# Optimization experiments

Hardware: AMD Instinct MI355X
Metric: run time of the kernel (lower is better)

## Reference

```python
import jax, jax.numpy as jnp
import numpy as np

N = 100000      # nodes
E = 1600000     # directed edges (avg degree 16)
DIN, DH, DOUT = 128, 128, 64


def gcn_conv(x, W, b, src, dst, n):
    """PyG GCNConv: out = D^{-1/2} (A + I) D^{-1/2} (x @ W) + b.
    src/dst already include self-loops."""
    deg = jax.ops.segment_sum(jnp.ones_like(src, dtype=x.dtype), dst, num_segments=n)
    dinv = jnp.where(deg > 0, jax.lax.rsqrt(deg), jnp.zeros_like(deg))
    norm = dinv[src] * dinv[dst]                      # [E+N]
    h = x @ W                                         # [N, dout] linear first (PyG)
    msg = h[src] * norm[:, None]                      # gather + scale, [E+N, dout]
    return jax.ops.segment_sum(msg, dst, num_segments=n) + b


def setup_inputs() -> dict:
    key = jax.random.key(0)
    k1, k2, k3 = jax.random.split(key, 3)
    x = jax.random.normal(k1, (N, DIN), dtype=jnp.float32)
    edge_index = jax.random.randint(k2, (2, E), 0, N, dtype=jnp.int64)
    kw1, kw2 = jax.random.split(k3)
    # glorot-style init for the two GCN linear weights
    W1 = jax.random.normal(kw1, (DIN, DH), dtype=jnp.float32) * (1.0 / np.sqrt(DIN))
    b1 = jnp.zeros((DH,), dtype=jnp.float32)
    W2 = jax.random.normal(kw2, (DH, DOUT), dtype=jnp.float32) * (1.0 / np.sqrt(DH))
    b2 = jnp.zeros((DOUT,), dtype=jnp.float32)
    return {"x": x, "W1": W1, "b1": b1, "W2": W2, "b2": b2, "edge_index": edge_index}


def reference(x, W1, b1, W2, b2, edge_index):
    n = x.shape[0]
    loops = jnp.arange(n, dtype=edge_index.dtype)
    src = jnp.concatenate([edge_index[0], loops])     # add self-loops
    dst = jnp.concatenate([edge_index[1], loops])
    h = jax.nn.relu(gcn_conv(x, W1, b1, src, dst, n))
    return gcn_conv(h, W2, b2, src, dst, n)
```

## Files before the change

### kernel.cpp

```cpp
#include <hip/hip_runtime.h>

#define N_NODES 100000
#define N_EDGES 1600000
#define BUCKET_SHIFT 7
#define NB 782
#define BIN_BLOCKS 782
#define GEMM_BLOCKS 1563
#define BCAP 2816
#define AGG1_BLOCKS 6250
#define AGG2_BLOCKS 3125

typedef short bf16x8 __attribute__((ext_vector_type(8)));
typedef float f32x4 __attribute__((ext_vector_type(4)));
typedef float f32x8 __attribute__((ext_vector_type(8)));

__device__ __forceinline__ unsigned short f2bf(float f) {
    unsigned int u = __float_as_uint(f);
    unsigned int r = (u + 0x7FFFu + ((u >> 16) & 1u)) >> 16;
    return (unsigned short)r;
}
__device__ __forceinline__ float bf2f(unsigned short b) {
    return __uint_as_float(((unsigned int)b) << 16);
}
__device__ __forceinline__ void acc8(float* a, uint4 v) {
    a[0] += __uint_as_float(v.x << 16);
    a[1] += __uint_as_float(v.x & 0xFFFF0000u);
    a[2] += __uint_as_float(v.y << 16);
    a[3] += __uint_as_float(v.y & 0xFFFF0000u);
    a[4] += __uint_as_float(v.z << 16);
    a[5] += __uint_as_float(v.z & 0xFFFF0000u);
    a[6] += __uint_as_float(v.w << 16);
    a[7] += __uint_as_float(v.w & 0xFFFF0000u);
}

__global__ __launch_bounds__(256) void k_tw(const float* __restrict__ W1, const float* __restrict__ W2,
                                            unsigned short* __restrict__ w1t, unsigned short* __restrict__ w2t,
                                            int* __restrict__ bcur) {
    int t = blockIdx.x * 256 + threadIdx.x;
    if (t < 16384) {
        int k = t >> 7, c = t & 127;
        w1t[c * 128 + k] = f2bf(W1[t]);
    } else if (t < 24576) {
        int i = t - 16384;
        int k = i >> 6, c = i & 63;
        w2t[c * 128 + k] = f2bf(W2[i]);
    } else if (t - 24576 < NB) {
        bcur[t - 24576] = 0;
    }
}

__global__ __launch_bounds__(256) void k_bin(const int* __restrict__ src, const int* __restrict__ dst,
                                             int* __restrict__ bcur, int* __restrict__ ebuf) {
    __shared__ int hist[NB];
    __shared__ int lbase[NB];
    int t = threadIdx.x;
    int e0 = blockIdx.x * 2048 + t;
    int s[8], d[8];
#pragma unroll
    for (int j = 0; j < 8; ++j) {
        int e = e0 + j * 256;
        bool ok = e < N_EDGES;
        s[j] = ok ? src[e] : -1;
        d[j] = ok ? dst[e] : 0;
    }
    for (int i = t; i < NB; i += 256) hist[i] = 0;
    __syncthreads();
#pragma unroll
    for (int j = 0; j < 8; ++j)
        if (s[j] >= 0) atomicAdd(&hist[d[j] >> BUCKET_SHIFT], 1);
    __syncthreads();
    for (int i = t; i < NB; i += 256)
        if (hist[i] > 0) lbase[i] = atomicAdd(&bcur[i], hist[i]);
    __syncthreads();
    for (int i = t; i < NB; i += 256) hist[i] = 0;
    __syncthreads();
#pragma unroll
    for (int j = 0; j < 8; ++j) {
        if (s[j] >= 0) {
            int b = d[j] >> BUCKET_SHIFT;
            int r = lbase[b] + atomicAdd(&hist[b], 1);
            if (r < BCAP) ebuf[b * BCAP + r] = ((d[j] & 127) << 17) | s[j];
        }
    }
}

__global__ __launch_bounds__(1024) void k_scan(const int* __restrict__ bcur, int* __restrict__ bbase,
                                               int* __restrict__ rowptr) {
    __shared__ int sc[1024];
    int t = threadIdx.x;
    int v = (t < NB) ? bcur[t] : 0;
    sc[t] = v;
    __syncthreads();
    for (int off = 1; off < 1024; off <<= 1) {
        int u = (t >= off) ? sc[t - off] : 0;
        __syncthreads();
        sc[t] += u;
        __syncthreads();
    }
    if (t < NB) bbase[t] = sc[t] - v;
    if (t == 0) rowptr[N_NODES] = N_EDGES;
}

__global__ __launch_bounds__(256) void k_bfill3(const int* __restrict__ ebuf, const int* __restrict__ bcur,
                                                const int* __restrict__ bbase,
                                                int* __restrict__ rowptr, float* __restrict__ dinv,
                                                int* __restrict__ csr) {
    __shared__ int cnt[128];
    __shared__ int sc[128];
    __shared__ int cur[128];
    int b = blockIdx.x, t = threadIdx.x;
    int node0 = b << BUCKET_SHIFT;
    if (t < 128) cnt[t] = 0;
    int cb = bcur[b];
    int s0 = bbase[b];
    int ctot = cb > BCAP ? BCAP : cb;
    const int* eb = ebuf + b * BCAP;
    __syncthreads();
    for (int i = t; i < ctot; i += 256) atomicAdd(&cnt[eb[i] >> 17], 1);
    __syncthreads();
    int c = (t < 128) ? cnt[t] : 0;
    if (t < 128) sc[t] = c;
    __syncthreads();
    for (int off = 1; off < 128; off <<= 1) {
        int u = (t < 128 && t >= off) ? sc[t - off] : 0;
        __syncthreads();
        if (t < 128) sc[t] += u;
        __syncthreads();
    }
    if (t < 128) {
        int p = s0 + sc[t] - c;
        int n = node0 + t;
        if (n < N_NODES) { rowptr[n] = p; dinv[n] = rsqrtf(1.0f + (float)c); }
        cur[t] = p;
    }
    __syncthreads();
    for (int i = t; i < ctot; i += 256) {
        int e = eb[i];
        int p = atomicAdd(&cur[e >> 17], 1);
        csr[p] = e & 0x1FFFF;
    }
}

__global__ __launch_bounds__(256) void k_gemm1(const float* __restrict__ x, const unsigned short* __restrict__ w1t,
                                               const float* __restrict__ dinv, unsigned short* __restrict__ hsb) {
    __shared__ unsigned short Xl[64 * 136];
    __shared__ unsigned short Wl[128 * 136];
    int t = threadIdx.x;
    int row0 = blockIdx.x * 64;
    for (int i = t; i < 64 * 32; i += 256) {
        int r = i >> 5, c4 = i & 31;
        int row = row0 + r;
        float4 v = (row < N_NODES) ? ((const float4*)x)[(long long)row * 32 + c4]
                                   : make_float4(0.f, 0.f, 0.f, 0.f);
        ushort4 o;
        o.x = f2bf(v.x); o.y = f2bf(v.y); o.z = f2bf(v.z); o.w = f2bf(v.w);
        *(ushort4*)&Xl[r * 136 + c4 * 4] = o;
    }
    for (int i = t; i < 128 * 16; i += 256) {
        int r = i >> 4, c8 = i & 15;
        *(bf16x8*)&Wl[r * 136 + c8 * 8] = *(const bf16x8*)&w1t[r * 128 + c8 * 8];
    }
    __syncthreads();
    int w = t >> 6, lane = t & 63;
    int nn = lane & 15, quad = lane >> 4;
    bf16x8 a[4];
#pragma unroll
    for (int kt = 0; kt < 4; ++kt)
        a[kt] = *(const bf16x8*)&Xl[(w * 16 + nn) * 136 + kt * 32 + quad * 8];
    f32x4 acc[8];
#pragma unroll
    for (int ct = 0; ct < 8; ++ct) {
        acc[ct] = (f32x4){0.f, 0.f, 0.f, 0.f};
#pragma unroll
        for (int kt = 0; kt < 4; ++kt) {
            bf16x8 b = *(const bf16x8*)&Wl[(ct * 16 + nn) * 136 + kt * 32 + quad * 8];
            acc[ct] = __builtin_amdgcn_mfma_f32_16x16x32_bf16(a[kt], b, acc[ct], 0, 0, 0);
        }
    }
#pragma unroll
    for (int r = 0; r < 4; ++r) {
        int row = row0 + w * 16 + quad * 4 + r;
        float dv = (row < N_NODES) ? dinv[row] : 0.f;
#pragma unroll
        for (int ct = 0; ct < 8; ++ct)
            Xl[(w * 16 + quad * 4 + r) * 136 + ct * 16 + nn] = f2bf(acc[ct][r] * dv);
    }
#pragma unroll
    for (int j = 0; j < 8; ++j) {
        int c = lane + j * 64;
        int r = c >> 5, c4 = c & 31;
        int row = row0 + w * 16 + r;
        if (row < N_NODES)
            ((ushort4*)(hsb + (long long)row * 128))[c4] = *(const ushort4*)&Xl[(w * 16 + r) * 136 + c4 * 4];
    }
}

__global__ __launch_bounds__(256) void k_agg1(const unsigned short* __restrict__ hsb, const int* __restrict__ rowptr,
                                              const int* __restrict__ csr, const float* __restrict__ dinv,
                                              const float* __restrict__ b1, unsigned short* __restrict__ h) {
    unsigned g = (blockIdx.x * 256 + threadIdx.x) >> 4;
    unsigned li = threadIdx.x & 15;
    if (g >= N_NODES) return;
    unsigned co = li * 8;
    float a[8];
    {
        uint4 sv = *(const uint4*)(hsb + (g << 7) + co);
        a[0] = __uint_as_float(sv.x << 16);
        a[1] = __uint_as_float(sv.x & 0xFFFF0000u);
        a[2] = __uint_as_float(sv.y << 16);
        a[3] = __uint_as_float(sv.y & 0xFFFF0000u);
        a[4] = __uint_as_float(sv.z << 16);
        a[5] = __uint_as_float(sv.z & 0xFFFF0000u);
        a[6] = __uint_as_float(sv.w << 16);
        a[7] = __uint_as_float(sv.w & 0xFFFF0000u);
    }
    int k = rowptr[g], end = rowptr[g + 1];
    for (; k + 7 < end; k += 8) {
        int i0 = csr[k + 0], i1 = csr[k + 1], i2 = csr[k + 2], i3 = csr[k + 3];
        int i4 = csr[k + 4], i5 = csr[k + 5], i6 = csr[k + 6], i7 = csr[k + 7];
        uint4 v0 = *(const uint4*)(hsb + (((unsigned)i0) << 7) + co);
        uint4 v1 = *(const uint4*)(hsb + (((unsigned)i1) << 7) + co);
        uint4 v2 = *(const uint4*)(hsb + (((unsigned)i2) << 7) + co);
        uint4 v3 = *(const uint4*)(hsb + (((unsigned)i3) << 7) + co);
        uint4 v4 = *(const uint4*)(hsb + (((unsigned)i4) << 7) + co);
        uint4 v5 = *(const uint4*)(hsb + (((unsigned)i5) << 7) + co);
        uint4 v6 = *(const uint4*)(hsb + (((unsigned)i6) << 7) + co);
        uint4 v7 = *(const uint4*)(hsb + (((unsigned)i7) << 7) + co);
        acc8(a, v0); acc8(a, v1); acc8(a, v2); acc8(a, v3);
        acc8(a, v4); acc8(a, v5); acc8(a, v6); acc8(a, v7);
    }
    if (k + 3 < end) {
        int i0 = csr[k + 0], i1 = csr[k + 1], i2 = csr[k + 2], i3 = csr[k + 3];
        uint4 v0 = *(const uint4*)(hsb + (((unsigned)i0) << 7) + co);
        uint4 v1 = *(const uint4*)(hsb + (((unsigned)i1) << 7) + co);
        uint4 v2 = *(const uint4*)(hsb + (((unsigned)i2) << 7) + co);
        uint4 v3 = *(const uint4*)(hsb + (((unsigned)i3) << 7) + co);
        acc8(a, v0); acc8(a, v1); acc8(a, v2); acc8(a, v3);
        k += 4;
    }
    for (; k < end; ++k) {
        uint4 v = *(const uint4*)(hsb + (((unsigned)csr[k]) << 7) + co);
        acc8(a, v);
    }
    float dv = dinv[g];
    f32x8 bb = *(const f32x8*)(b1 + li * 8);
    bf16x8 o;
#pragma unroll
    for (int j = 0; j < 8; ++j)
        o[j] = (short)f2bf(fmaxf(fmaf(dv, a[j], bb[j]), 0.f));
    *(bf16x8*)(h + (g << 7) + co) = o;
}

__global__ __launch_bounds__(256) void k_gemm2(const unsigned short* __restrict__ h, const unsigned short* __restrict__ w2t,
                                               const float* __restrict__ dinv, unsigned short* __restrict__ gsb) {
    __shared__ unsigned short Hl[64 * 136];
    __shared__ unsigned short Wl[64 * 136];
    int t = threadIdx.x;
    int row0 = blockIdx.x * 64;
    for (int i = t; i < 64 * 16; i += 256) {
        int r = i >> 4, c8 = i & 15;
        int row = row0 + r;
        bf16x8 v = (row < N_NODES) ? *(const bf16x8*)&h[(long long)row * 128 + c8 * 8]
                                   : (bf16x8){0, 0, 0, 0, 0, 0, 0, 0};
        *(bf16x8*)&Hl[r * 136 + c8 * 8] = v;
        *(bf16x8*)&Wl[r * 136 + c8 * 8] = *(const bf16x8*)&w2t[r * 128 + c8 * 8];
    }
    __syncthreads();
    int w = t >> 6, lane = t & 63;
    int nn = lane & 15, quad = lane >> 4;
    bf16x8 a[4];
#pragma unroll
    for (int kt = 0; kt < 4; ++kt)
        a[kt] = *(const bf16x8*)&Hl[(w * 16 + nn) * 136 + kt * 32 + quad * 8];
    f32x4 acc[4];
#pragma unroll
    for (int ct = 0; ct < 4; ++ct) {
        acc[ct] = (f32x4){0.f, 0.f, 0.f, 0.f};
#pragma unroll
        for (int kt = 0; kt < 4; ++kt) {
            bf16x8 b = *(const bf16x8*)&Wl[(ct * 16 + nn) * 136 + kt * 32 + quad * 8];
            acc[ct] = __builtin_amdgcn_mfma_f32_16x16x32_bf16(a[kt], b, acc[ct], 0, 0, 0);
        }
    }
#pragma unroll
    for (int r = 0; r < 4; ++r) {
        int row = row0 + w * 16 + quad * 4 + r;
        float dv = (row < N_NODES) ? dinv[row] : 0.f;
#pragma unroll
        for (int ct = 0; ct < 4; ++ct)
            Hl[(w * 16 + quad * 4 + r) * 136 + ct * 16 + nn] = f2bf(acc[ct][r] * dv);
    }
#pragma unroll
    for (int j = 0; j < 4; ++j) {
        int c = lane + j * 64;
        int r = c >> 4, c4 = c & 15;
        int row = row0 + w * 16 + r;
        if (row < N_NODES)
            ((ushort4*)(gsb + (long long)row * 64))[c4] = *(const ushort4*)&Hl[(w * 16 + r) * 136 + c4 * 4];
    }
}

__global__ __launch_bounds__(256) void k_agg2(const unsigned short* __restrict__ gsb, const int* __restrict__ rowptr,
                                              const int* __restrict__ csr, const float* __restrict__ dinv,
                                              const float* __restrict__ b2, float* __restrict__ out) {
    unsigned g = (blockIdx.x * 256 + threadIdx.x) >> 3;
    unsigned li = threadIdx.x & 7;
    if (g >= N_NODES) return;
    unsigned co = li * 8;
    float a[8];
    {
        uint4 sv = *(const uint4*)(gsb + (g << 6) + co);
        a[0] = __uint_as_float(sv.x << 16);
        a[1] = __uint_as_float(sv.x & 0xFFFF0000u);
        a[2] = __uint_as_float(sv.y << 16);
        a[3] = __uint_as_float(sv.y & 0xFFFF0000u);
        a[4] = __uint_as_float(sv.z << 16);
        a[5] = __uint_as_float(sv.z & 0xFFFF0000u);
        a[6] = __uint_as_float(sv.w << 16);
        a[7] = __uint_as_float(sv.w & 0xFFFF0000u);
    }
    int k = rowptr[g], end = rowptr[g + 1];
    for (; k + 7 < end; k += 8) {
        int i0 = csr[k + 0], i1 = csr[k + 1], i2 = csr[k + 2], i3 = csr[k + 3];
        int i4 = csr[k + 4], i5 = csr[k + 5], i6 = csr[k + 6], i7 = csr[k + 7];
        uint4 v0 = *(const uint4*)(gsb + (((unsigned)i0) << 6) + co);
        uint4 v1 = *(const uint4*)(gsb + (((unsigned)i1) << 6) + co);
        uint4 v2 = *(const uint4*)(gsb + (((unsigned)i2) << 6) + co);
        uint4 v3 = *(const uint4*)(gsb + (((unsigned)i3) << 6) + co);
        uint4 v4 = *(const uint4*)(gsb + (((unsigned)i4) << 6) + co);
        uint4 v5 = *(const uint4*)(gsb + (((unsigned)i5) << 6) + co);
        uint4 v6 = *(const uint4*)(gsb + (((unsigned)i6) << 6) + co);
        uint4 v7 = *(const uint4*)(gsb + (((unsigned)i7) << 6) + co);
        acc8(a, v0); acc8(a, v1); acc8(a, v2); acc8(a, v3);
        acc8(a, v4); acc8(a, v5); acc8(a, v6); acc8(a, v7);
    }
    if (k + 3 < end) {
        int i0 = csr[k + 0], i1 = csr[k + 1], i2 = csr[k + 2], i3 = csr[k + 3];
        uint4 v0 = *(const uint4*)(gsb + (((unsigned)i0) << 6) + co);
        uint4 v1 = *(const uint4*)(gsb + (((unsigned)i1) << 6) + co);
        uint4 v2 = *(const uint4*)(gsb + (((unsigned)i2) << 6) + co);
        uint4 v3 = *(const uint4*)(gsb + (((unsigned)i3) << 6) + co);
        acc8(a, v0); acc8(a, v1); acc8(a, v2); acc8(a, v3);
        k += 4;
    }
    for (; k < end; ++k) {
        uint4 v = *(const uint4*)(gsb + (((unsigned)csr[k]) << 6) + co);
        acc8(a, v);
    }
    float dv = dinv[g];
    f32x8 bb = *(const f32x8*)(b2 + li * 8);
    float4 o0 = make_float4(fmaf(dv, a[0], bb[0]), fmaf(dv, a[1], bb[1]),
                            fmaf(dv, a[2], bb[2]), fmaf(dv, a[3], bb[3]));
    float4 o1 = make_float4(fmaf(dv, a[4], bb[4]), fmaf(dv, a[5], bb[5]),
                            fmaf(dv, a[6], bb[6]), fmaf(dv, a[7], bb[7]));
    float* op = out + ((long long)g << 6) + co;
    *(float4*)op = o0;
    *(float4*)(op + 4) = o1;
}

extern "C" void kernel_launch(void* const* d_in, const int* in_sizes, int n_in,
                              void* d_out, int out_size, void* d_ws, size_t ws_size,
                              hipStream_t stream) {
    const float* x  = (const float*)d_in[0];
    const float* W1 = (const float*)d_in[1];
    const float* b1 = (const float*)d_in[2];
    const float* W2 = (const float*)d_in[3];
    const float* b2 = (const float*)d_in[4];
    const int*   ei = (const int*)d_in[5];
    const int* src = ei;
    const int* dst = ei + N_EDGES;
    float* out = (float*)d_out;

    char* ws = (char*)d_ws;
    int*   csr    = (int*)(ws + 0);
    int*   rowptr = (int*)(ws + 6800000);
    float* dinv   = (float*)(ws + 7200256);
    int*   bcur   = (int*)(ws + 7604352);
    unsigned short* w1t = (unsigned short*)(ws + 7608448);
    unsigned short* w2t = (unsigned short*)(ws + 7641216);
    int*   bbase  = (int*)(ws + 7657600);
    int*   ebuf   = (int*)(ws + 8388608);
    unsigned short* hsb = (unsigned short*)(ws + 8388608);
    unsigned short* h   = (unsigned short*)(ws + 59588608);
    unsigned short* gsb = hsb;

    k_tw<<<100, 256, 0, stream>>>(W1, W2, w1t, w2t, bcur);
    k_bin<<<BIN_BLOCKS, 256, 0, stream>>>(src, dst, bcur, ebuf);
    k_scan<<<1, 1024, 0, stream>>>(bcur, bbase, rowptr);
    k_bfill3<<<NB, 256, 0, stream>>>(ebuf, bcur, bbase, rowptr, dinv, csr);

    k_gemm1<<<GEMM_BLOCKS, 256, 0, stream>>>(x, w1t, dinv, hsb);
    k_agg1<<<AGG1_BLOCKS, 256, 0, stream>>>(hsb, rowptr, csr, dinv, b1, h);
    k_gemm2<<<GEMM_BLOCKS, 256, 0, stream>>>(h, w2t, dinv, gsb);
    k_agg2<<<AGG2_BLOCKS, 256, 0, stream>>>(gsb, rowptr, csr, dinv, b2, out);
}
```

Measured before the change: 271.7 us.

## Replace bucket scan kernel with atomic offset claim and store (start,count) rows

Drops the single-block k_scan launch. Each bfill block now claims its CSR segment base with an atomicAdd on a global counter, so bucket segments land in arbitrary order. Rows are stored as a (start, count) pair, so aggregation no longer reads rowptr[g+1]. The layer-1 aggregation is also split into two launches of half the nodes each, which adds a launch and does not obviously help.

```diff
diff --git a/kernel.cpp b/kernel.cpp
--- a/kernel.cpp
+++ b/kernel.cpp
@@ -7,7 +7,7 @@
 #define BIN_BLOCKS 782
 #define GEMM_BLOCKS 1563
 #define BCAP 2816
-#define AGG1_BLOCKS 6250
+#define AGG1_BLOCKS 3125
 #define AGG2_BLOCKS 3125
 
 typedef short bf16x8 __attribute__((ext_vector_type(8)));
@@ -35,7 +35,7 @@
 
 __global__ __launch_bounds__(256) void k_tw(const float* __restrict__ W1, const float* __restrict__ W2,
                                             unsigned short* __restrict__ w1t, unsigned short* __restrict__ w2t,
-                                            int* __restrict__ bcur) {
+                                            int* __restrict__ bcur, int* __restrict__ gcount) {
     int t = blockIdx.x * 256 + threadIdx.x;
     if (t < 16384) {
         int k = t >> 7, c = t & 127;
@@ -46,6 +46,8 @@
         w2t[c * 128 + k] = f2bf(W2[i]);
     } else if (t - 24576 < NB) {
         bcur[t - 24576] = 0;
+    } else if (t - 24576 == NB) {
+        *gcount = 0;
     }
 }
 
@@ -84,36 +86,20 @@
     }
 }
 
-__global__ __launch_bounds__(1024) void k_scan(const int* __restrict__ bcur, int* __restrict__ bbase,
-                                               int* __restrict__ rowptr) {
-    __shared__ int sc[1024];
-    int t = threadIdx.x;
-    int v = (t < NB) ? bcur[t] : 0;
-    sc[t] = v;
-    __syncthreads();
-    for (int off = 1; off < 1024; off <<= 1) {
-        int u = (t >= off) ? sc[t - off] : 0;
-        __syncthreads();
-        sc[t] += u;
-        __syncthreads();
-    }
-    if (t < NB) bbase[t] = sc[t] - v;
-    if (t == 0) rowptr[N_NODES] = N_EDGES;
-}
-
 __global__ __launch_bounds__(256) void k_bfill3(const int* __restrict__ ebuf, const int* __restrict__ bcur,
-                                                const int* __restrict__ bbase,
-                                                int* __restrict__ rowptr, float* __restrict__ dinv,
+                                                int* __restrict__ gcount,
+                                                uint2* __restrict__ rowptr2, float* __restrict__ dinv,
                                                 int* __restrict__ csr) {
     __shared__ int cnt[128];
     __shared__ int sc[128];
     __shared__ int cur[128];
+    __shared__ int s0s;
     int b = blockIdx.x, t = threadIdx.x;
     int node0 = b << BUCKET_SHIFT;
     if (t < 128) cnt[t] = 0;
     int cb = bcur[b];
-    int s0 = bbase[b];
     int ctot = cb > BCAP ? BCAP : cb;
+    if (t == 0) s0s = atomicAdd(gcount, ctot);
     const int* eb = ebuf + b * BCAP;
     __syncthreads();
     for (int i = t; i < ctot; i += 256) atomicAdd(&cnt[eb[i] >> 17], 1);
@@ -127,10 +113,11 @@
         if (t < 128) sc[t] += u;
         __syncthreads();
     }
+    int s0 = s0s;
     if (t < 128) {
         int p = s0 + sc[t] - c;
         int n = node0 + t;
-        if (n < N_NODES) { rowptr[n] = p; dinv[n] = rsqrtf(1.0f + (float)c); }
+        if (n < N_NODES) { rowptr2[n] = make_uint2((unsigned)p, (unsigned)c); dinv[n] = rsqrtf(1.0f + (float)c); }
         cur[t] = p;
     }
     __syncthreads();
@@ -195,10 +182,11 @@
     }
 }
 
-__global__ __launch_bounds__(256) void k_agg1(const unsigned short* __restrict__ hsb, const int* __restrict__ rowptr,
+__global__ __launch_bounds__(256) void k_agg1(const unsigned short* __restrict__ hsb, const uint2* __restrict__ rowptr2,
                                               const int* __restrict__ csr, const float* __restrict__ dinv,
-                                              const float* __restrict__ b1, unsigned short* __restrict__ h) {
-    unsigned g = (blockIdx.x * 256 + threadIdx.x) >> 4;
+                                              const float* __restrict__ b1, unsigned short* __restrict__ h,
+                                              int base) {
+    unsigned g = base + ((blockIdx.x * 256 + threadIdx.x) >> 4);
     unsigned li = threadIdx.x & 15;
     if (g >= N_NODES) return;
     unsigned co = li * 8;
@@ -214,7 +202,8 @@
         a[6] = __uint_as_float(sv.w << 16);
         a[7] = __uint_as_float(sv.w & 0xFFFF0000u);
     }
-    int k = rowptr[g], end = rowptr[g + 1];
+    uint2 rp = rowptr2[g];
+    int k = (int)rp.x, end = (int)(rp.x + rp.y);
     for (; k + 7 < end; k += 8) {
         int i0 = csr[k + 0], i1 = csr[k + 1], i2 = csr[k + 2], i3 = csr[k + 3];
         int i4 = csr[k + 4], i5 = csr[k + 5], i6 = csr[k + 6], i7 = csr[k + 7];
@@ -300,7 +289,7 @@
     }
 }
 
-__global__ __launch_bounds__(256) void k_agg2(const unsigned short* __restrict__ gsb, const int* __restrict__ rowptr,
+__global__ __launch_bounds__(256) void k_agg2(const unsigned short* __restrict__ gsb, const uint2* __restrict__ rowptr2,
                                               const int* __restrict__ csr, const float* __restrict__ dinv,
                                               const float* __restrict__ b2, float* __restrict__ out) {
     unsigned g = (blockIdx.x * 256 + threadIdx.x) >> 3;
@@ -319,7 +308,8 @@
         a[6] = __uint_as_float(sv.w << 16);
         a[7] = __uint_as_float(sv.w & 0xFFFF0000u);
     }
-    int k = rowptr[g], end = rowptr[g + 1];
+    uint2 rp = rowptr2[g];
+    int k = (int)rp.x, end = (int)(rp.x + rp.y);
     for (; k + 7 < end; k += 8) {
         int i0 = csr[k + 0], i1 = csr[k + 1], i2 = csr[k + 2], i3 = csr[k + 3];
         int i4 = csr[k + 4], i5 = csr[k + 5], i6 = csr[k + 6], i7 = csr[k + 7];
@@ -372,25 +362,25 @@
     float* out = (float*)d_out;
 
     char* ws = (char*)d_ws;
-    int*   csr    = (int*)(ws + 0);
-    int*   rowptr = (int*)(ws + 6800000);
-    float* dinv   = (float*)(ws + 7200256);
-    int*   bcur   = (int*)(ws + 7604352);
+    int*   csr     = (int*)(ws + 0);
+    uint2* rowptr2 = (uint2*)(ws + 6400000);
+    float* dinv    = (float*)(ws + 7200000);
+    int*   bcur    = (int*)(ws + 7600000);
+    int*   gcount  = (int*)(ws + 7603200);
     unsigned short* w1t = (unsigned short*)(ws + 7608448);
     unsigned short* w2t = (unsigned short*)(ws + 7641216);
-    int*   bbase  = (int*)(ws + 7657600);
-    int*   ebuf   = (int*)(ws + 8388608);
+    int*   ebuf    = (int*)(ws + 8388608);
     unsigned short* hsb = (unsigned short*)(ws + 8388608);
     unsigned short* h   = (unsigned short*)(ws + 59588608);
     unsigned short* gsb = hsb;
 
-    k_tw<<<100, 256, 0, stream>>>(W1, W2, w1t, w2t, bcur);
+    k_tw<<<100, 256, 0, stream>>>(W1, W2, w1t, w2t, bcur, gcount);
     k_bin<<<BIN_BLOCKS, 256, 0, stream>>>(src, dst, bcur, ebuf);
-    k_scan<<<1, 1024, 0, stream>>>(bcur, bbase, rowptr);
-    k_bfill3<<<NB, 256, 0, stream>>>(ebuf, bcur, bbase, rowptr, dinv, csr);
+    k_bfill3<<<NB, 256, 0, stream>>>(ebuf, bcur, gcount, rowptr2, dinv, csr);
 
     k_gemm1<<<GEMM_BLOCKS, 256, 0, stream>>>(x, w1t, dinv, hsb);
-    k_agg1<<<AGG1_BLOCKS, 256, 0, stream>>>(hsb, rowptr, csr, dinv, b1, h);
+    k_agg1<<<AGG1_BLOCKS, 256, 0, stream>>>(hsb, rowptr2, csr, dinv, b1, h, 0);
+    k_agg1<<<AGG1_BLOCKS, 256, 0, stream>>>(hsb, rowptr2, csr, dinv, b1, h, 50000);
     k_gemm2<<<GEMM_BLOCKS, 256, 0, stream>>>(h, w2t, dinv, gsb);
-    k_agg2<<<AGG2_BLOCKS, 256, 0, stream>>>(gsb, rowptr, csr, dinv, b2, out);
-}
+    k_agg2<<<AGG2_BLOCKS, 256, 0, stream>>>(gsb, rowptr2, csr, dinv, b2, out);
+}
```

Measured after the change: 286.2 us. 1.05x slower.
